# Kernel tuning notes

Hardware: AMD Instinct MI355X
Metric: run time of the kernel (lower is better)

The kernel has to match this reference:

```python
import jax, jax.numpy as jnp
import numpy as np

NI = 50000      # input nodes
NO = 50000      # output nodes
DEG = 16        # uniform neighborhood size -> E = NO*DEG
E = NO * DEG
FI = 64         # input feature dim
UNITS = 64
D = 3           # coord feature dim


def setup_inputs() -> dict:
    key = jax.random.key(0)
    k1, k2, k3, k4 = jax.random.split(key, 4)
    node_features = jax.random.normal(k1, (NI, FI), dtype=jnp.float32)
    coord_features = jax.random.normal(k2, (E, D), dtype=jnp.float32)
    indices = jax.random.randint(k3, (E,), 0, NI, dtype=jnp.int64)
    # uniform ragged structure: each output node has DEG edges
    row_splits = (jnp.arange(NO + 1, dtype=jnp.int64) * DEG)
    W = jax.random.normal(k4, (FI, UNITS * D), dtype=jnp.float32) * (1.0 / np.sqrt(FI))
    b = jnp.zeros((UNITS * D,), dtype=jnp.float32)
    return {"node_features": node_features, "coord_features": coord_features,
            "indices": indices, "row_splits": row_splits, "W": W, "b": b}


def reference(node_features, coord_features, indices, row_splits, W, b):
    # Dense projection on input nodes: [Ni, units*D]
    h = node_features @ W + b
    # gather_first=False path of ragged_convolution_transpose: gather after dense
    g = h[indices]                       # [E, units*D]
    g = g.reshape(-1, UNITS, D)          # [E, units, D]
    # contract over coord dim: f_eu = sum_d g_eud * coord_ed
    f = jnp.einsum('eud,ed->eu', g, coord_features)  # [E, units]
    # activation is None (identity)
    # ragged segment-sum via row_splits -> segment ids per edge
    num_out = row_splits.shape[0] - 1
    row_lengths = jnp.diff(row_splits)
    seg_ids = jnp.repeat(jnp.arange(num_out), row_lengths,
                         total_repeat_length=f.shape[0])
    out = jax.ops.segment_sum(f, seg_ids, num_segments=num_out)  # [No, units]
    return out
```

## Files before the change

kernel.cpp:

```cpp
#include <hip/hip_runtime.h>


#define NO 50000
#define DEG 16
#define FI 64
#define UNITS 64
#define KK 192
#define TN 16
#define NSTEP 6
#define GPAD 200
#define NBLK 1536
#define NTILES (NO / TN)

typedef __attribute__((ext_vector_type(8))) short short8;
typedef __attribute__((ext_vector_type(4))) float float4v;

static __device__ __forceinline__ unsigned int asu(float x){ union{float f;unsigned int u;}c; c.f=x; return c.u; }
static __device__ __forceinline__ float asf(unsigned int x){ union{unsigned int u;float f;}c; c.u=x; return c.f; }
static __device__ __forceinline__ float rdlane_f(float v, int l){
    return asf((unsigned int)__builtin_amdgcn_readlane((int)asu(v), l));
}

__global__ __launch_bounds__(256, 6)
void rct3(const float* __restrict__ nf, const float* __restrict__ coord,
          const int* __restrict__ idx, const float* __restrict__ W,
          const float* __restrict__ b, float* __restrict__ out)
{
    __shared__ __align__(16) unsigned short Ghi[2][TN][GPAD];
    __shared__ __align__(16) unsigned short Glo[2][TN][GPAD];
    __shared__ __align__(16) float Cs[2][TN][4];

    const int tid  = threadIdx.x;
    const int w    = tid >> 6;
    const int lane = tid & 63;
    const int m16  = lane & 15;
    const int quad = lane >> 4;

    const int u = 16 * w + m16;
    short8 Bf[NSTEP];
    #pragma unroll
    for (int s = 0; s < NSTEP; ++s) {
        #pragma unroll
        for (int j = 0; j < 8; ++j) {
            const int k = s * 32 + quad * 8 + j;
            const int i = k / 3, d = k - 3 * i;
            const float v = W[i * KK + 3 * u + d];
            const unsigned int vb = asu(v);
            const unsigned int rh = (vb + 0x7FFFu + ((vb >> 16) & 1u)) >> 16;
            Bf[s][j] = (short)rh;
        }
    }
    const float b0 = b[3*u+0], b1 = b[3*u+1], b2 = b[3*u+2];

    int t = blockIdx.x;
    int   vid;
    float cv0, cv1, cv2;
    {
        const int e = (t * TN + 4 * w) * DEG + lane;
        vid = __builtin_nontemporal_load(&idx[e]);
        cv0 = __builtin_nontemporal_load(&coord[3*e+0]);
        cv1 = __builtin_nontemporal_load(&coord[3*e+1]);
        cv2 = __builtin_nontemporal_load(&coord[3*e+2]);
    }

    int pp = 0;
    for (; t < NTILES; t += NBLK, pp ^= 1) {
        const int node0 = t * TN;

        const int t2 = t + NBLK;
        int   vidN = 0;
        float cv0N = 0.f, cv1N = 0.f, cv2N = 0.f;
        if (t2 < NTILES) {
            const int e2 = (t2 * TN + 4 * w) * DEG + lane;
            vidN = __builtin_nontemporal_load(&idx[e2]);
            cv0N = __builtin_nontemporal_load(&coord[3*e2+0]);
            cv1N = __builtin_nontemporal_load(&coord[3*e2+1]);
            cv2N = __builtin_nontemporal_load(&coord[3*e2+2]);
        }

        {
            float s0 = cv0, s1 = cv1, s2 = cv2;
            #pragma unroll
            for (int m = 1; m <= 8; m <<= 1) {
                s0 += __shfl_xor(s0, m, 64);
                s1 += __shfl_xor(s1, m, 64);
                s2 += __shfl_xor(s2, m, 64);
            }
            if ((lane & 15) == 0) {
                float4v cc = {s0, s1, s2, 0.f};
                *(float4v*)(&Cs[pp][4*w + (lane >> 4)][0]) = cc;
            }
        }

        #pragma unroll
        for (int r = 0; r < 4; ++r) {
            const int n = 4 * w + r;
            float a0 = 0.f, a1 = 0.f, a2 = 0.f;
            #pragma unroll
            for (int j = 0; j < DEG; ++j) {
                const int l  = 16 * r + j;
                const int id = __builtin_amdgcn_readlane(vid, l);
                const float c0 = rdlane_f(cv0, l);
                const float c1 = rdlane_f(cv1, l);
                const float c2 = rdlane_f(cv2, l);
                const float v  = nf[id * FI + lane];
                a0 += v * c0; a1 += v * c1; a2 += v * c2;
            }
            const unsigned int x0 = asu(a0), x1 = asu(a1), x2 = asu(a2);
            Ghi[pp][n][3*lane+0] = (unsigned short)(x0 >> 16);
            Ghi[pp][n][3*lane+1] = (unsigned short)(x1 >> 16);
            Ghi[pp][n][3*lane+2] = (unsigned short)(x2 >> 16);
            Glo[pp][n][3*lane+0] = (unsigned short)(asu(a0 - asf(x0 & 0xFFFF0000u)) >> 16);
            Glo[pp][n][3*lane+1] = (unsigned short)(asu(a1 - asf(x1 & 0xFFFF0000u)) >> 16);
            Glo[pp][n][3*lane+2] = (unsigned short)(asu(a2 - asf(x2 & 0xFFFF0000u)) >> 16);
        }
        __syncthreads();

        float4v acc = {0.f, 0.f, 0.f, 0.f};
        #pragma unroll
        for (int s = 0; s < NSTEP; ++s) {
            const short8 Ahi = *(const short8*)(&Ghi[pp][m16][s*32 + quad*8]);
            const short8 Alo = *(const short8*)(&Glo[pp][m16][s*32 + quad*8]);
            acc = __builtin_amdgcn_mfma_f32_16x16x32_bf16(Ahi, Bf[s], acc, 0, 0, 0);
            acc = __builtin_amdgcn_mfma_f32_16x16x32_bf16(Alo, Bf[s], acc, 0, 0, 0);
        }

        #pragma unroll
        for (int reg = 0; reg < 4; ++reg) {
            const int row = quad * 4 + reg;
            const float4v c = *(const float4v*)(&Cs[pp][row][0]);
            out[(node0 + row) * UNITS + u] =
                acc[reg] + c[0]*b0 + c[1]*b1 + c[2]*b2;
        }

        vid = vidN; cv0 = cv0N; cv1 = cv1N; cv2 = cv2N;
    }
}

extern "C" void kernel_launch(void* const* d_in, const int* in_sizes, int n_in,
                              void* d_out, int out_size, void* d_ws, size_t ws_size,
                              hipStream_t stream) {
    const float* nf    = (const float*)d_in[0];
    const float* coord = (const float*)d_in[1];
    const int*   idx   = (const int*)d_in[2];
    const float* W     = (const float*)d_in[4];
    const float* b     = (const float*)d_in[5];
    float* out = (float*)d_out;

    rct3<<<dim3(NBLK), dim3(256), 0, stream>>>(nf, coord, idx, W, b, out);
}
```

Baseline: 108.9 us.

## Gather node features from bf16 copy and drop split-bf16 MFMA pass

Adds a pre-pass kernel that converts node features to bf16 in workspace, so the random gather in the main kernel moves half the bytes. The per-node aggregates are now rounded to a single bf16 value instead of a hi/lo pair, which halves the MFMA work and the shared-memory footprint. Grid size and occupancy hint change to match. This lowers numerical precision: both the gathered features and the aggregates lose low mantissa bits, which risks exceeding tolerance. It also adds an extra kernel launch and a full read/write pass over the features.

Result: no change. 108.0 us (-0.8%).

```diff
diff --git a/kernel.cpp b/kernel.cpp
--- a/kernel.cpp
+++ b/kernel.cpp
@@ -2,6 +2,7 @@
 
 
 #define NO 50000
+#define NI 50000
 #define DEG 16
 #define FI 64
 #define UNITS 64
@@ -9,25 +10,43 @@
 #define TN 16
 #define NSTEP 6
 #define GPAD 200
-#define NBLK 1536
+#define NBLK 1024
 #define NTILES (NO / TN)
+#define NFELEM (NI * FI)
 
 typedef __attribute__((ext_vector_type(8))) short short8;
 typedef __attribute__((ext_vector_type(4))) float float4v;
+typedef __attribute__((ext_vector_type(4))) unsigned short ushort4v;
 
 static __device__ __forceinline__ unsigned int asu(float x){ union{float f;unsigned int u;}c; c.f=x; return c.u; }
 static __device__ __forceinline__ float asf(unsigned int x){ union{unsigned int u;float f;}c; c.u=x; return c.f; }
 static __device__ __forceinline__ float rdlane_f(float v, int l){
     return asf((unsigned int)__builtin_amdgcn_readlane((int)asu(v), l));
 }
+static __device__ __forceinline__ unsigned short f2bf_rne(float x){
+    const unsigned int v = asu(x);
+    return (unsigned short)((v + 0x7FFFu + ((v >> 16) & 1u)) >> 16);
+}
 
-__global__ __launch_bounds__(256, 6)
-void rct3(const float* __restrict__ nf, const float* __restrict__ coord,
-          const int* __restrict__ idx, const float* __restrict__ W,
-          const float* __restrict__ b, float* __restrict__ out)
+__global__ __launch_bounds__(256)
+void rct3_cvt(const float* __restrict__ nf, unsigned short* __restrict__ nf16)
+{
+    const int i = blockIdx.x * 256 + threadIdx.x;
+    const float4v v = ((const float4v*)nf)[i];
+    ushort4v o;
+    o[0] = f2bf_rne(v[0]); o[1] = f2bf_rne(v[1]);
+    o[2] = f2bf_rne(v[2]); o[3] = f2bf_rne(v[3]);
+    ((ushort4v*)nf16)[i] = o;
+}
+
+template<bool BF16>
+__global__ __launch_bounds__(256, 4)
+void rct3(const float* __restrict__ nf, const unsigned short* __restrict__ nf16,
+          const float* __restrict__ coord, const int* __restrict__ idx,
+          const float* __restrict__ W, const float* __restrict__ b,
+          float* __restrict__ out)
 {
     __shared__ __align__(16) unsigned short Ghi[2][TN][GPAD];
-    __shared__ __align__(16) unsigned short Glo[2][TN][GPAD];
     __shared__ __align__(16) float Cs[2][TN][4];
 
     const int tid  = threadIdx.x;
@@ -44,10 +63,7 @@
         for (int j = 0; j < 8; ++j) {
             const int k = s * 32 + quad * 8 + j;
             const int i = k / 3, d = k - 3 * i;
-            const float v = W[i * KK + 3 * u + d];
-            const unsigned int vb = asu(v);
-            const unsigned int rh = (vb + 0x7FFFu + ((vb >> 16) & 1u)) >> 16;
-            Bf[s][j] = (short)rh;
+            Bf[s][j] = (short)f2bf_rne(W[i * KK + 3 * u + d]);
         }
     }
     const float b0 = b[3*u+0], b1 = b[3*u+1], b2 = b[3*u+2];
@@ -103,16 +119,17 @@
                 const float c0 = rdlane_f(cv0, l);
                 const float c1 = rdlane_f(cv1, l);
                 const float c2 = rdlane_f(cv2, l);
-                const float v  = nf[id * FI + lane];
+                float v;
+                if constexpr (BF16) {
+                    v = asf(((unsigned int)nf16[id * FI + lane]) << 16);
+                } else {
+                    v = nf[id * FI + lane];
+                }
                 a0 += v * c0; a1 += v * c1; a2 += v * c2;
             }
-            const unsigned int x0 = asu(a0), x1 = asu(a1), x2 = asu(a2);
-            Ghi[pp][n][3*lane+0] = (unsigned short)(x0 >> 16);
-            Ghi[pp][n][3*lane+1] = (unsigned short)(x1 >> 16);
-            Ghi[pp][n][3*lane+2] = (unsigned short)(x2 >> 16);
-            Glo[pp][n][3*lane+0] = (unsigned short)(asu(a0 - asf(x0 & 0xFFFF0000u)) >> 16);
-            Glo[pp][n][3*lane+1] = (unsigned short)(asu(a1 - asf(x1 & 0xFFFF0000u)) >> 16);
-            Glo[pp][n][3*lane+2] = (unsigned short)(asu(a2 - asf(x2 & 0xFFFF0000u)) >> 16);
+            Ghi[pp][n][3*lane+0] = f2bf_rne(a0);
+            Ghi[pp][n][3*lane+1] = f2bf_rne(a1);
+            Ghi[pp][n][3*lane+2] = f2bf_rne(a2);
         }
         __syncthreads();
 
@@ -120,9 +137,7 @@
         #pragma unroll
         for (int s = 0; s < NSTEP; ++s) {
             const short8 Ahi = *(const short8*)(&Ghi[pp][m16][s*32 + quad*8]);
-            const short8 Alo = *(const short8*)(&Glo[pp][m16][s*32 + quad*8]);
             acc = __builtin_amdgcn_mfma_f32_16x16x32_bf16(Ahi, Bf[s], acc, 0, 0, 0);
-            acc = __builtin_amdgcn_mfma_f32_16x16x32_bf16(Alo, Bf[s], acc, 0, 0, 0);
         }
 
         #pragma unroll
@@ -147,5 +162,13 @@
     const float* b     = (const float*)d_in[5];
     float* out = (float*)d_out;
 
-    rct3<<<dim3(NBLK), dim3(256), 0, stream>>>(nf, coord, idx, W, b, out);
+    if (ws_size >= (size_t)NFELEM * sizeof(unsigned short)) {
+        unsigned short* nf16 = (unsigned short*)d_ws;
+        rct3_cvt<<<dim3(NFELEM / 4 / 256), dim3(256), 0, stream>>>(nf, nf16);
+        rct3<true><<<dim3(NBLK), dim3(256), 0, stream>>>(
+            nf, nf16, coord, idx, W, b, out);
+    } else {
+        rct3<false><<<dim3(NBLK), dim3(256), 0, stream>>>(
+            nf, nullptr, coord, idx, W, b, out);
+    }
 }
```
